# Kernel tuning notes

Measured on AMD Instinct MI355X. Metric: run time of the kernel, lower is better.

Reference implementation:

```python
import jax, jax.numpy as jnp
import numpy as np

B, S, D, H, DFF = 2, 2048, 1024, 16, 4096
DK = D // H


def _layer_norm(x, g, b, eps=1e-5):
    mu = jnp.mean(x, axis=-1, keepdims=True)
    var = jnp.mean((x - mu) ** 2, axis=-1, keepdims=True)
    return (x - mu) / jnp.sqrt(var + eps) * g + b


def setup_inputs() -> dict:
    key = jax.random.key(0)
    ks = jax.random.split(key, 12)
    w = lambda k, shape: jax.random.normal(k, shape, jnp.float32) * 0.02
    return {
        "x": jax.random.normal(ks[0], (B, S, D), jnp.float32),
        "mask": jnp.tril(jnp.ones((1, 1, S, S), jnp.int32)),  # causal tgt mask
        "Wq": w(ks[1], (D, D)), "bq": jnp.zeros((D,), jnp.float32),
        "Wk": w(ks[2], (D, D)), "bk": jnp.zeros((D,), jnp.float32),
        "Wv": w(ks[3], (D, D)), "bv": jnp.zeros((D,), jnp.float32),
        "Wo": w(ks[4], (D, D)), "bo": jnp.zeros((D,), jnp.float32),
        "W1": w(ks[5], (D, DFF)), "b1": jnp.zeros((DFF,), jnp.float32),
        "W2": w(ks[6], (DFF, D)), "b2": jnp.zeros((D,), jnp.float32),
        "g1": jnp.ones((D,), jnp.float32), "be1": jnp.zeros((D,), jnp.float32),
        "g2": jnp.ones((D,), jnp.float32), "be2": jnp.zeros((D,), jnp.float32),
    }


def reference(x, mask, Wq, bq, Wk, bk, Wv, bv, Wo, bo, W1, b1, W2, b2, g1, be1, g2, be2):
    b, s, d = x.shape
    h, dk = H, DK
    split = lambda t: t.reshape(b, s, h, dk).transpose(0, 2, 1, 3)  # [b,h,s,dk]
    q = split(x @ Wq + bq)
    k = split(x @ Wk + bk)
    v = split(x @ Wv + bv)
    scores = jnp.einsum("bhqd,bhkd->bhqk", q, k) / jnp.sqrt(jnp.float32(dk))
    # ALiBi: slope_h = (2**(8/H))**-(h+1); bias[h,i,j] = slope_h * (j - i)
    slopes = (2.0 ** (8.0 / h)) ** (-jnp.arange(1, h + 1, dtype=jnp.float32))
    rel = (jnp.arange(s)[None, :] - jnp.arange(s)[:, None]).astype(jnp.float32)
    scores = scores + slopes[:, None, None] * rel[None]  # [1? broadcast b,h,s,s]
    scores = jnp.where(mask == 0, jnp.float32(-1e9), scores)
    probs = jax.nn.softmax(scores, axis=-1)
    attn = jnp.einsum("bhqk,bhkd->bhqd", probs, v)
    attn = attn.transpose(0, 2, 1, 3).reshape(b, s, d) @ Wo + bo
    x = _layer_norm(x + attn, g1, be1)
    ff = jax.nn.relu(x @ W1 + b1) @ W2 + b2
    return _layer_norm(x + ff, g2, be2)
```

## Files before the change

kernel.cpp:

```cpp
#include <hip/hip_runtime.h>
#include <stdint.h>

typedef unsigned short u16;
typedef __bf16 bf16x8 __attribute__((ext_vector_type(8)));
typedef float f32x4 __attribute__((ext_vector_type(4)));
typedef float f32x16 __attribute__((ext_vector_type(16)));
typedef unsigned int uint2v __attribute__((ext_vector_type(2)));

#define S_LEN 2048
#define D_MODEL 1024

struct TrueT  { static constexpr bool value = true;  };
struct FalseT { static constexpr bool value = false; };

__device__ __forceinline__ u16 f2b(float f) {
    uint32_t u = __float_as_uint(f);
    u += 0x7FFFu + ((u >> 16) & 1u);
    return (u16)(u >> 16);
}

__device__ __forceinline__ uint32_t pk2(float a, float b) {
    union { struct { __bf16 l, h; } s; uint32_t u; } c;
    c.s.l = (__bf16)a; c.s.h = (__bf16)b; return c.u;
}

__device__ __forceinline__ float fexp2(float x) {
#if __has_builtin(__builtin_amdgcn_exp2f)
    return __builtin_amdgcn_exp2f(x);
#else
    return exp2f(x);
#endif
}

__device__ __forceinline__ uint2v plswap(uint32_t a, uint32_t b) {
#if __has_builtin(__builtin_amdgcn_permlane32_swap)
    return __builtin_amdgcn_permlane32_swap(a, b, false, false);
#else
    uint2v r;
    uint32_t pa = (uint32_t)__shfl_xor((int)a, 32, 64);
    uint32_t pb = (uint32_t)__shfl_xor((int)b, 32, 64);
    const int hi = (threadIdx.x & 63) >> 5;
    r[0] = hi ? pb : a;
    r[1] = hi ? b : pa;
    return r;
#endif
}
__device__ __forceinline__ float xhalf_max(float x) {
    uint2v r = plswap(__float_as_uint(x), __float_as_uint(x));
    return fmaxf(__uint_as_float(r[0]), __uint_as_float(r[1]));
}
__device__ __forceinline__ float xhalf_add(float x) {
    uint2v r = plswap(__float_as_uint(x), __float_as_uint(x));
    return __uint_as_float(r[0]) + __uint_as_float(r[1]);
}

__device__ __forceinline__ void gl16(const void* g, void* l) {
    __builtin_amdgcn_global_load_lds(
        (const __attribute__((address_space(1))) void*)g,
        (__attribute__((address_space(3))) void*)l, 16, 0, 0);
}

__global__ __launch_bounds__(256) void k_convert_bf16(
    const float* __restrict__ in, u16* __restrict__ out, int n)
{
    int i = (blockIdx.x * 256 + threadIdx.x) * 4;
    if (i >= n) return;
    float4 v = *reinterpret_cast<const float4*>(in + i);
    ushort4 o;
    o.x = f2b(v.x); o.y = f2b(v.y); o.z = f2b(v.z); o.w = f2b(v.w);
    *reinterpret_cast<ushort4*>(out + i) = o;
}

__global__ __launch_bounds__(256) void k_transpose_w(
    const float* __restrict__ W, u16* __restrict__ WT, int K, int N)
{
    __shared__ float tile[32][33];
    const int nt = blockIdx.x, kt = blockIdx.y;
    const int tx = threadIdx.x & 31, ty = threadIdx.x >> 5;
#pragma unroll
    for (int i = 0; i < 4; ++i)
        tile[ty + i * 8][tx] = W[(long)(kt * 32 + ty + i * 8) * N + nt * 32 + tx];
    __syncthreads();
#pragma unroll
    for (int i = 0; i < 4; ++i)
        WT[(long)(nt * 32 + ty + i * 8) * K + kt * 32 + tx] = f2b(tile[tx][ty + i * 8]);
}

template <int MODE>
__global__ __launch_bounds__(256) void k_gemm(
    const u16* __restrict__ A, const u16* __restrict__ BT,
    const float* __restrict__ bias, const float* __restrict__ bias2,
    const float* __restrict__ bias3,
    u16* __restrict__ outb, float* __restrict__ outf,
    int M, int N, int K, int va, int vb)
{
    __shared__ u16 As[2][128 * 32];
    __shared__ u16 Bs[2][128 * 32];
    const int t = threadIdx.x;
    const int lane = t & 63, wid = t >> 6;
    const int wm = wid >> 1, wn = wid & 1;
    const int lr = lane & 15, lg = lane >> 4;

    const int GX = gridDim.x, GY = gridDim.y;
    const int dd = blockIdx.y * GX + blockIdx.x;
    const int xcd = dd & 7, ii = dd >> 3;
    const int hb = GY / va, wb = GX / vb;
    const int pr = xcd / vb, pc = xcd % vb;
    const int by = pr * hb + ii / wb;
    const int bx = pc * wb + ii % wb;
    const int m0 = by * 128, n0 = bx * 128;

    const int Kc = K / (int)gridDim.z;
    const long koff = (long)blockIdx.z * Kc;

    f32x4 acc[4][4];
#pragma unroll
    for (int i = 0; i < 4; ++i)
#pragma unroll
        for (int j = 0; j < 4; ++j) acc[i][j] = (f32x4){0.f, 0.f, 0.f, 0.f};

    const int r0 = t >> 2;
    const int ce = (t & 3) * 8;
    const u16* pA0 = A + (long)(m0 + r0) * K + ce + koff;
    const u16* pA1 = A + (long)(m0 + r0 + 64) * K + ce + koff;
    const u16* pB0 = BT + (long)(n0 + r0) * K + ce + koff;
    const u16* pB1 = BT + (long)(n0 + r0 + 64) * K + ce + koff;

    auto STAGE = [&](int buf, int k0) {
        u16* aw = &As[buf][wid * 512];
        u16* bw = &Bs[buf][wid * 512];
        gl16(pA0 + k0, aw);
        gl16(pA1 + k0, aw + 2048);
        gl16(pB0 + k0, bw);
        gl16(pB1 + k0, bw + 2048);
    };

    STAGE(0, 0);
    __syncthreads();
    int cur = 0;
    for (int k0 = 0; k0 < Kc; k0 += 32) {
        if (k0 + 32 < Kc) STAGE(cur ^ 1, k0 + 32);
        bf16x8 af[4], bfr[4];
#pragma unroll
        for (int i = 0; i < 4; ++i)
            af[i] = *reinterpret_cast<const bf16x8*>(&As[cur][(wm * 64 + i * 16 + lr) * 32 + lg * 8]);
#pragma unroll
        for (int j = 0; j < 4; ++j)
            bfr[j] = *reinterpret_cast<const bf16x8*>(&Bs[cur][(wn * 64 + j * 16 + lr) * 32 + lg * 8]);
#pragma unroll
        for (int i = 0; i < 4; ++i)
#pragma unroll
            for (int j = 0; j < 4; ++j)
                acc[i][j] = __builtin_amdgcn_mfma_f32_16x16x32_bf16(af[i], bfr[j], acc[i][j], 0, 0, 0);
        __syncthreads();
        cur ^= 1;
    }

    const long zoff = (long)blockIdx.z * M * N;
#pragma unroll
    for (int i = 0; i < 4; ++i) {
#pragma unroll
        for (int j = 0; j < 4; ++j) {
            const int n = n0 + wn * 64 + j * 16 + lr;
            float bn = 0.f;
            if (MODE == 0)
                bn = (n < 1024) ? bias[n] : (n < 2048) ? bias2[n - 1024] : bias3[n - 2048];
            else if (MODE == 2)
                bn = bias[n];
#pragma unroll
            for (int r = 0; r < 4; ++r) {
                const int m = m0 + wm * 64 + i * 16 + lg * 4 + r;
                float v = acc[i][j][r] + bn;
                if (MODE == 0) {
                    const int b = m >> 11, s = m & 2047;
                    const int which = n >> 10, nn = n & 1023;
                    const int h = nn >> 6, dk = nn & 63;
                    const long bhb = (long)(b * 16 + h) * (2048L * 64);
                    const int s32 = s >> 5, sr = s & 31;
                    long addr;
                    if (which < 2) {
                        addr = bhb + (long)s32 * 2048 + (dk >> 4) * 512 +
                               ((dk >> 3) & 1) * 256 + sr * 8 + (dk & 7);
                    } else {
                        addr = bhb + (long)s32 * 2048 + (dk >> 5) * 1024 +
                               ((sr >> 4) & 1) * 512 + ((sr >> 3) & 1) * 256 +
                               (dk & 31) * 8 + (sr & 7);
                    }
                    outb[(long)which * (32L * 2048 * 64) + addr] = f2b(v);
                } else if (MODE == 2) {
                    outb[(long)m * N + n] = f2b(fmaxf(v, 0.f));
                } else {
                    outf[zoff + (long)m * N + n] = v;
                }
            }
        }
    }
}

__global__ __launch_bounds__(256, 3) void k_attn4(
    const u16* __restrict__ qg, const u16* __restrict__ kg,
    const u16* __restrict__ vtg, u16* __restrict__ attnb)
{
    __shared__ float Ol[4][32][68];
    __shared__ float Ml[4][32];
    __shared__ float Ll[4][32];

    const int t = threadIdx.x;
    const int lane = t & 63, w = t >> 6;
    const int qc = lane & 31, hi = lane >> 5;
    const int bid = blockIdx.x;
    const int xcd = bid & 7, slot = bid >> 3;
    const int bh = xcd * 4 + (slot & 3);
    const int pr = slot >> 2;
    const int b = bh >> 4, h = bh & 15;
    const float slope2 = fexp2(-0.5f * (float)(h + 1)) * 1.44269504f;
    const float SC = 0.18033688f;
    const long base = (long)bh * (S_LEN * 64L);

    const u16* kptr = kg + base + lane * 8;
    const u16* vptr = vtg + base + lane * 8;
    const u16* qptr = qg + base + lane * 8;

#define LOADK(S, DST) {                                                   \
        const u16* kr_ = kptr + (long)(S) * 2048;                         \
        DST[0] = *reinterpret_cast<const bf16x8*>(kr_);                   \
        DST[1] = *reinterpret_cast<const bf16x8*>(kr_ + 512);             \
        DST[2] = *reinterpret_cast<const bf16x8*>(kr_ + 1024);            \
        DST[3] = *reinterpret_cast<const bf16x8*>(kr_ + 1536); }

    for (int pi = 0; pi < 2; ++pi) {
        const int qt = pi ? pr : 63 - pr;
        const int q_abs = qt * 32 + qc;

        bf16x8 qf[4];
        {
            const u16* qt_ = qptr + (long)qt * 2048;
#pragma unroll
            for (int ds = 0; ds < 4; ++ds)
                qf[ds] = *reinterpret_cast<const bf16x8*>(qt_ + ds * 512);
        }

        f32x16 oacc[2];
#pragma unroll
        for (int i = 0; i < 16; ++i) { oacc[0][i] = 0.f; oacc[1][i] = 0.f; }
        float m = -1e30f, l = 0.f;

        const int nsub = qt + 1;
        const int L = (nsub + 3) >> 2;
        const int s_beg = w * L;
        const int s_end = min(s_beg + L, nsub);
        const bool has_diag = (s_beg < s_end) && (s_end == nsub);
        const int e_un = has_diag ? s_end - 1 : s_end;

        bf16x8 kf[4];

        auto SUBTILE = [&](int s, int nxt, auto MASKC) {
            constexpr bool MASK = decltype(MASKC)::value;
            const int k0 = s * 32;
            f32x16 st;
#pragma unroll
            for (int i = 0; i < 16; ++i) st[i] = 0.f;
#pragma unroll
            for (int ds = 0; ds < 4; ++ds)
                st = __builtin_amdgcn_mfma_f32_32x32x16_bf16(kf[ds], qf[ds], st, 0, 0, 0);
            if (nxt >= 0) LOADK(nxt, kf);
            bf16x8 vf[2][2];
            {
                const u16* vt_ = vptr + (long)s * 2048;
#pragma unroll
                for (int dh = 0; dh < 2; ++dh)
#pragma unroll
                    for (int ks = 0; ks < 2; ++ks)
                        vf[dh][ks] = *reinterpret_cast<const bf16x8*>(
                            vt_ + dh * 1024 + ks * 512);
            }

            const float b0 = slope2 * (float)(k0 - q_abs + 4 * hi);
#pragma unroll
            for (int r = 0; r < 16; ++r) {
                const int roff = (r & 3) + 8 * (r >> 2);
                float xx = fmaf(st[r], SC, fmaf((float)roff, slope2, b0));
                if (MASK) {
                    const int kabs = k0 + roff + 4 * hi;
                    xx = (kabs > q_abs) ? -1e30f : xx;
                }
                st[r] = xx;
            }
            float mt[8];
#pragma unroll
            for (int r = 0; r < 8; ++r) mt[r] = fmaxf(st[2 * r], st[2 * r + 1]);
#pragma unroll
            for (int r = 0; r < 4; ++r) mt[r] = fmaxf(mt[r], mt[r + 4]);
            mt[0] = fmaxf(mt[0], mt[2]); mt[1] = fmaxf(mt[1], mt[3]);
            float mloc = xhalf_max(fmaxf(mt[0], mt[1]));

            if (!__all(mloc <= m + 11.5416f)) {
                const float mnew = fmaxf(m, mloc);
                const float corr = fexp2(m - mnew);
                m = mnew;
                l *= corr;
#pragma unroll
                for (int i = 0; i < 16; ++i) { oacc[0][i] *= corr; oacc[1][i] *= corr; }
            }

#pragma unroll
            for (int r = 0; r < 16; ++r) st[r] = fexp2(st[r] - m);
            float pt[8];
#pragma unroll
            for (int r = 0; r < 8; ++r) pt[r] = st[2 * r] + st[2 * r + 1];
#pragma unroll
            for (int r = 0; r < 4; ++r) pt[r] = pt[r] + pt[r + 4];
            pt[0] += pt[2]; pt[1] += pt[3];
            l += xhalf_add(pt[0] + pt[1]);

            bf16x8 pa[2];
#pragma unroll
            for (int g2 = 0; g2 < 2; ++g2) {
                uint32_t o0 = pk2(st[8 * g2 + 0], st[8 * g2 + 1]);
                uint32_t o1 = pk2(st[8 * g2 + 2], st[8 * g2 + 3]);
                uint32_t o2 = pk2(st[8 * g2 + 4], st[8 * g2 + 5]);
                uint32_t o3 = pk2(st[8 * g2 + 6], st[8 * g2 + 7]);
                uint2v ra = plswap(o0, o2);
                uint2v rb = plswap(o1, o3);
                union { uint32_t wd[4]; bf16x8 v; } c;
                c.wd[0] = ra[0]; c.wd[1] = rb[0]; c.wd[2] = ra[1]; c.wd[3] = rb[1];
                pa[g2] = c.v;
            }
#pragma unroll
            for (int ks = 0; ks < 2; ++ks)
#pragma unroll
                for (int dh = 0; dh < 2; ++dh)
                    oacc[dh] = __builtin_amdgcn_mfma_f32_32x32x16_bf16(vf[dh][ks], pa[ks], oacc[dh], 0, 0, 0);
        };

        int s = s_beg;
        if (s < s_end) LOADK(s, kf);
        for (; s < e_un; ++s)
            SUBTILE(s, (s + 1 < s_end) ? s + 1 : -1, FalseT{});
        if (has_diag)
            SUBTILE(qt, -1, TrueT{});

#pragma unroll
        for (int dh = 0; dh < 2; ++dh)
#pragma unroll
            for (int g = 0; g < 4; ++g) {
                float4 o4 = make_float4(oacc[dh][4 * g + 0], oacc[dh][4 * g + 1],
                                        oacc[dh][4 * g + 2], oacc[dh][4 * g + 3]);
                *reinterpret_cast<float4*>(&Ol[w][qc][dh * 32 + g * 8 + hi * 4]) = o4;
            }
        if (hi == 0) { Ml[w][qc] = m; Ll[w][qc] = l; }
        __syncthreads();

        {
            const int q = t >> 3, dg = t & 7;
            const float m0v = Ml[0][q], m1v = Ml[1][q], m2v = Ml[2][q], m3v = Ml[3][q];
            const float M = fmaxf(fmaxf(m0v, m1v), fmaxf(m2v, m3v));
            float wgt[4];
            wgt[0] = fexp2(m0v - M); wgt[1] = fexp2(m1v - M);
            wgt[2] = fexp2(m2v - M); wgt[3] = fexp2(m3v - M);
            const float lsum = wgt[0] * Ll[0][q] + wgt[1] * Ll[1][q] +
                               wgt[2] * Ll[2][q] + wgt[3] * Ll[3][q];
            float acc8[8];
#pragma unroll
            for (int e = 0; e < 8; ++e) acc8[e] = 0.f;
#pragma unroll
            for (int w4 = 0; w4 < 4; ++w4) {
                const float wg = wgt[w4];
#pragma unroll
                for (int e = 0; e < 8; ++e)
                    acc8[e] += wg * Ol[w4][q][dg * 8 + e];
            }
            const float inv = 1.0f / lsum;
            u16 ob[8];
#pragma unroll
            for (int e = 0; e < 8; ++e) ob[e] = f2b(acc8[e] * inv);
            *reinterpret_cast<uint4*>(
                &attnb[((long)b * S_LEN + qt * 32 + q) * 1024 + h * 64 + dg * 8]) =
                *reinterpret_cast<uint4*>(&ob[0]);
        }
        __syncthreads();
    }
#undef LOADK
}

__global__ __launch_bounds__(256) void k_ln(
    const float* __restrict__ P0, const float* __restrict__ P1,
    const float* __restrict__ resid, const float* __restrict__ pbias,
    const float* __restrict__ g, const float* __restrict__ be,
    float* __restrict__ outf, u16* __restrict__ outb, int writeb)
{
    __shared__ float red[2][4];
    const int row = blockIdx.x, t = threadIdx.x;
    const long o = (long)row * 1024 + t * 4;
    float4 a0 = *reinterpret_cast<const float4*>(P0 + o);
    float4 a1 = *reinterpret_cast<const float4*>(P1 + o);
    float4 rr = *reinterpret_cast<const float4*>(resid + o);
    float4 pb = *reinterpret_cast<const float4*>(pbias + t * 4);
    float4 vv;
    vv.x = a0.x + a1.x + rr.x + pb.x;
    vv.y = a0.y + a1.y + rr.y + pb.y;
    vv.z = a0.z + a1.z + rr.z + pb.z;
    vv.w = a0.w + a1.w + rr.w + pb.w;
    float s = vv.x + vv.y + vv.z + vv.w;
    float sq = vv.x * vv.x + vv.y * vv.y + vv.z * vv.z + vv.w * vv.w;
#pragma unroll
    for (int off = 1; off < 64; off <<= 1) {
        s += __shfl_xor(s, off, 64);
        sq += __shfl_xor(sq, off, 64);
    }
    const int w = t >> 6;
    if ((t & 63) == 0) { red[0][w] = s; red[1][w] = sq; }
    __syncthreads();
    s = red[0][0] + red[0][1] + red[0][2] + red[0][3];
    sq = red[1][0] + red[1][1] + red[1][2] + red[1][3];
    const float mu = s * (1.f / 1024.f);
    const float var = sq * (1.f / 1024.f) - mu * mu;
    const float rs = rsqrtf(var + 1e-5f);
    float4 gv = *reinterpret_cast<const float4*>(&g[t * 4]);
    float4 bv = *reinterpret_cast<const float4*>(&be[t * 4]);
    float4 ov;
    ov.x = (vv.x - mu) * rs * gv.x + bv.x;
    ov.y = (vv.y - mu) * rs * gv.y + bv.y;
    ov.z = (vv.z - mu) * rs * gv.z + bv.z;
    ov.w = (vv.w - mu) * rs * gv.w + bv.w;
    *reinterpret_cast<float4*>(&outf[o]) = ov;
    if (writeb) {
        ushort4 ob;
        ob.x = f2b(ov.x); ob.y = f2b(ov.y); ob.z = f2b(ov.z); ob.w = f2b(ov.w);
        *reinterpret_cast<ushort4*>(&outb[o]) = ob;
    }
}

extern "C" void kernel_launch(void* const* d_in, const int* in_sizes, int n_in,
                              void* d_out, int out_size, void* d_ws, size_t ws_size,
                              hipStream_t stream)
{
    const float* x  = (const float*)d_in[0];
    const float* Wq = (const float*)d_in[2];  const float* bq = (const float*)d_in[3];
    const float* Wk = (const float*)d_in[4];  const float* bk = (const float*)d_in[5];
    const float* Wv = (const float*)d_in[6];  const float* bv = (const float*)d_in[7];
    const float* Wo = (const float*)d_in[8];  const float* bo = (const float*)d_in[9];
    const float* W1 = (const float*)d_in[10]; const float* b1 = (const float*)d_in[11];
    const float* W2 = (const float*)d_in[12]; const float* b2 = (const float*)d_in[13];
    const float* g1 = (const float*)d_in[14]; const float* be1 = (const float*)d_in[15];
    const float* g2 = (const float*)d_in[16]; const float* be2 = (const float*)d_in[17];
    float* out = (float*)d_out;

    char* ws = (char*)d_ws;
    const size_t MB = 1 << 20;
    u16* XB   = (u16*)(ws + 0 * MB);
    u16* QKVT = (u16*)(ws + 8 * MB);
    u16* WOT  = (u16*)(ws + 14 * MB);
    u16* W1T  = (u16*)(ws + 16 * MB);
    u16* W2T  = (u16*)(ws + 96 * MB);
    u16* QKV  = (u16*)(ws + 32 * MB);
    u16* AT   = (u16*)(ws + 64 * MB);
    float* OP = (float*)(ws + 32 * MB);
    float* Y1 = (float*)(ws + 0 * MB);
    u16* Y1B  = (u16*)(ws + 64 * MB);
    u16* Hb   = (u16*)(ws + 24 * MB);
    float* FP = (float*)(ws + 56 * MB);

    u16* Qb = QKV;
    u16* Kb = QKV + 32L * 2048 * 64;
    u16* Vb = QKV + 2 * 32L * 2048 * 64;

    dim3 blk(256);

    k_convert_bf16<<<dim3(4096), blk, 0, stream>>>(x, XB, 4096 * 1024);
    k_transpose_w<<<dim3(32, 32), blk, 0, stream>>>(Wq, QKVT, 1024, 1024);
    k_transpose_w<<<dim3(32, 32), blk, 0, stream>>>(Wk, QKVT + 1024L * 1024, 1024, 1024);
    k_transpose_w<<<dim3(32, 32), blk, 0, stream>>>(Wv, QKVT + 2048L * 1024, 1024, 1024);
    k_transpose_w<<<dim3(32, 32), blk, 0, stream>>>(Wo, WOT, 1024, 1024);
    k_transpose_w<<<dim3(128, 32), blk, 0, stream>>>(W1, W1T, 1024, 4096);
    k_transpose_w<<<dim3(32, 128), blk, 0, stream>>>(W2, W2T, 4096, 1024);

    k_gemm<0><<<dim3(24, 32), blk, 0, stream>>>(XB, QKVT, bq, bk, bv,
                                                QKV, nullptr, 4096, 3072, 1024, 4, 2);

    k_attn4<<<dim3(1024), blk, 0, stream>>>(Qb, Kb, Vb, AT);

    k_gemm<1><<<dim3(8, 32, 2), blk, 0, stream>>>(AT, WOT, nullptr, nullptr, nullptr,
                                                  nullptr, OP, 4096, 1024, 1024, 4, 2);
    k_ln<<<dim3(4096), blk, 0, stream>>>(OP, OP + 4096L * 1024, x, bo,
                                         g1, be1, Y1, Y1B, 1);
    k_gemm<2><<<dim3(32, 32), blk, 0, stream>>>(Y1B, W1T, b1, nullptr, nullptr,
                                                Hb, nullptr, 4096, 4096, 1024, 2, 4);
    k_gemm<1><<<dim3(8, 32, 2), blk, 0, stream>>>(Hb, W2T, nullptr, nullptr, nullptr,
                                                  nullptr, FP, 4096, 1024, 4096, 4, 2);
    k_ln<<<dim3(4096), blk, 0, stream>>>(FP, FP + 4096L * 1024, Y1, b2,
                                         g2, be2, out, nullptr, 0);
}
```

Measured before the change: 245.9 us.

## Add 256x256-tile 8-wave GEMM with split-K LDS pipelining for FFN up-projection

Adds a new 512-thread GEMM kernel that computes 256x256 output tiles with 8 waves. Each 64-wide K step is split into two 32-wide halves held in double-buffered, XOR-swizzled LDS, and global-to-LDS loads are interleaved between the MFMA phases, which run at raised wave priority. The FFN W1 GEMM with bias+ReLU now uses this kernel instead of the 256-thread generic GEMM. The goal is more operand reuse per tile and better overlap of loads with MFMA. The cost is more registers and LDS per block and only 256 blocks in the grid.

Measured after the change: 234.1 us. 4.8% less time.

```diff
diff --git a/kernel.cpp b/kernel.cpp
--- a/kernel.cpp
+++ b/kernel.cpp
@@ -195,6 +195,141 @@
             }
         }
     }
+}
+
+__global__ __launch_bounds__(512, 2) void k_gemm8(
+    const u16* __restrict__ A, const u16* __restrict__ BT,
+    const float* __restrict__ bias, u16* __restrict__ outb,
+    int M, int N, int K, int va, int vb)
+{
+    __shared__ u16 As[2][2][8192];
+    __shared__ u16 Bs[2][2][8192];
+    const int t = threadIdx.x;
+    const int lane = t & 63, wid = t >> 6;
+    const int wm = wid >> 2, wn = wid & 3;
+    const int lr = lane & 15, lg = lane >> 4;
+
+    const int GX = gridDim.x, GY = gridDim.y;
+    const int dd = blockIdx.y * GX + blockIdx.x;
+    const int xcd = dd & 7, ii = dd >> 3;
+    const int hb = GY / va, wb = GX / vb;
+    const int by = (xcd / vb) * hb + ii / wb;
+    const int bx = (xcd % vb) * wb + ii % wb;
+    const int m0 = by * 256, n0 = bx * 256;
+
+    const int NT = K >> 6;
+
+    auto STAGEU = [&](const u16* __restrict__ P, int rbase, u16* lds_unit,
+                      int tt, int kh) {
+        const int ko = tt * 64 + kh * 32;
+#pragma unroll
+        for (int s = 0; s < 2; ++s) {
+            const int c = wid * 64 + lane + s * 512;
+            const int op = c * 16;
+            const int row = op >> 6;
+            const int kg = ((op >> 4) & 3) ^ (row & 3);
+            gl16(P + (long)(rbase + row) * K + ko + kg * 8,
+                 (char*)lds_unit + op);
+        }
+    };
+    auto RD = [&](const u16* unit, int rb) -> bf16x8 {
+        const int row = rb + lr;
+        const int op = (row * 64 + lg * 16) ^ ((row & 3) << 4);
+        return *reinterpret_cast<const bf16x8*>((const char*)unit + op);
+    };
+
+    f32x4 acc[8][4];
+#pragma unroll
+    for (int i = 0; i < 8; ++i)
+#pragma unroll
+        for (int j = 0; j < 4; ++j) acc[i][j] = (f32x4){0.f, 0.f, 0.f, 0.f};
+
+    STAGEU(A, m0, &As[0][0][0], 0, 0);
+    STAGEU(BT, n0, &Bs[0][0][0], 0, 0);
+    STAGEU(A, m0, &As[0][1][0], 0, 1);
+    STAGEU(BT, n0, &Bs[0][1][0], 0, 1);
+    STAGEU(A, m0, &As[1][0][0], 1, 0);
+    STAGEU(BT, n0, &Bs[1][0][0], 1, 0);
+    asm volatile("s_waitcnt vmcnt(0)" ::: "memory");
+    __builtin_amdgcn_s_barrier();
+
+    for (int tt = 0; tt < NT; ++tt) {
+        const int sl = tt & 1;
+        bf16x8 af[4], bfr[4];
+
+#pragma unroll
+        for (int rf = 0; rf < 4; ++rf)
+            af[rf] = RD(&As[sl][0][0], wm * 128 + rf * 16);
+#pragma unroll
+        for (int cf = 0; cf < 4; ++cf)
+            bfr[cf] = RD(&Bs[sl][0][0], wn * 64 + cf * 16);
+        if (tt + 1 < NT) STAGEU(A, m0, &As[sl ^ 1][1][0], tt + 1, 1);
+        __builtin_amdgcn_s_setprio(1);
+#pragma unroll
+        for (int cf = 0; cf < 4; ++cf)
+#pragma unroll
+            for (int rf = 0; rf < 4; ++rf)
+                acc[rf][cf] = __builtin_amdgcn_mfma_f32_16x16x32_bf16(af[rf], bfr[cf], acc[rf][cf], 0, 0, 0);
+        __builtin_amdgcn_s_setprio(0);
+        __builtin_amdgcn_s_barrier();
+
+#pragma unroll
+        for (int rf = 0; rf < 4; ++rf)
+            af[rf] = RD(&As[sl][0][0], wm * 128 + 64 + rf * 16);
+        if (tt + 1 < NT) STAGEU(BT, n0, &Bs[sl ^ 1][1][0], tt + 1, 1);
+        __builtin_amdgcn_s_setprio(1);
+#pragma unroll
+        for (int cf = 0; cf < 4; ++cf)
+#pragma unroll
+            for (int rf = 0; rf < 4; ++rf)
+                acc[4 + rf][cf] = __builtin_amdgcn_mfma_f32_16x16x32_bf16(af[rf], bfr[cf], acc[4 + rf][cf], 0, 0, 0);
+        __builtin_amdgcn_s_setprio(0);
+        asm volatile("s_waitcnt vmcnt(8)" ::: "memory");
+        __builtin_amdgcn_s_barrier();
+
+#pragma unroll
+        for (int rf = 0; rf < 4; ++rf)
+            af[rf] = RD(&As[sl][1][0], wm * 128 + rf * 16);
+#pragma unroll
+        for (int cf = 0; cf < 4; ++cf)
+            bfr[cf] = RD(&Bs[sl][1][0], wn * 64 + cf * 16);
+        if (tt + 2 < NT) STAGEU(A, m0, &As[sl][0][0], tt + 2, 0);
+        __builtin_amdgcn_s_setprio(1);
+#pragma unroll
+        for (int cf = 0; cf < 4; ++cf)
+#pragma unroll
+            for (int rf = 0; rf < 4; ++rf)
+                acc[rf][cf] = __builtin_amdgcn_mfma_f32_16x16x32_bf16(af[rf], bfr[cf], acc[rf][cf], 0, 0, 0);
+        __builtin_amdgcn_s_setprio(0);
+        __builtin_amdgcn_s_barrier();
+
+#pragma unroll
+        for (int rf = 0; rf < 4; ++rf)
+            af[rf] = RD(&As[sl][1][0], wm * 128 + 64 + rf * 16);
+        if (tt + 2 < NT) STAGEU(BT, n0, &Bs[sl][0][0], tt + 2, 0);
+        __builtin_amdgcn_s_setprio(1);
+#pragma unroll
+        for (int cf = 0; cf < 4; ++cf)
+#pragma unroll
+            for (int rf = 0; rf < 4; ++rf)
+                acc[4 + rf][cf] = __builtin_amdgcn_mfma_f32_16x16x32_bf16(af[rf], bfr[cf], acc[4 + rf][cf], 0, 0, 0);
+        __builtin_amdgcn_s_setprio(0);
+        asm volatile("s_waitcnt vmcnt(8)" ::: "memory");
+        __builtin_amdgcn_s_barrier();
+    }
+
+#pragma unroll
+    for (int fr = 0; fr < 8; ++fr)
+#pragma unroll
+        for (int cf = 0; cf < 4; ++cf) {
+            const int n = n0 + wn * 64 + cf * 16 + lr;
+            const float bn = bias[n];
+#pragma unroll
+            for (int r = 0; r < 4; ++r) {
+                const int m = m0 + wm * 128 + fr * 16 + lg * 4 + r;
+                outb[(long)m * N + n] = f2b(fmaxf(acc[fr][cf][r] + bn, 0.f));
+            }
+        }
 }
 
 __global__ __launch_bounds__(256, 3) void k_attn4(
@@ -484,8 +619,8 @@
                                                   nullptr, OP, 4096, 1024, 1024, 4, 2);
     k_ln<<<dim3(4096), blk, 0, stream>>>(OP, OP + 4096L * 1024, x, bo,
                                          g1, be1, Y1, Y1B, 1);
-    k_gemm<2><<<dim3(32, 32), blk, 0, stream>>>(Y1B, W1T, b1, nullptr, nullptr,
-                                                Hb, nullptr, 4096, 4096, 1024, 2, 4);
+    k_gemm8<<<dim3(16, 16), dim3(512), 0, stream>>>(Y1B, W1T, b1, Hb,
+                                                    4096, 4096, 1024, 2, 4);
     k_gemm<1><<<dim3(8, 32, 2), blk, 0, stream>>>(Hb, W2T, nullptr, nullptr, nullptr,
                                                   nullptr, FP, 4096, 1024, 4096, 4, 2);
     k_ln<<<dim3(4096), blk, 0, stream>>>(FP, FP + 4096L * 1024, Y1, b2,
```
